# Optimization experiments

Hardware: AMD Instinct MI355X
Metric: run time of the kernel (lower is better)

The kernel has to match this reference:

```python
import jax, jax.numpy as jnp
import numpy as np

B_SZ, L_MAX, T_LEN, D = 512, 48, 128, 300   # sentences, graph slots, tokens, glove_dim
N_A, N_C = 2048, 2048                        # aspect rows, clause rows
H, TOP_K = 4, 96                             # attention heads, top-k over flattened LxL


def setup_inputs() -> dict:
    key = jax.random.key(0)
    ks = jax.random.split(key, 8)
    input_embed = jax.random.normal(ks[0], (B_SZ, T_LEN, D), jnp.float32)
    clause_output = jax.random.normal(ks[1], (N_C, D), jnp.float32)
    batch_aa_mask = (jax.random.uniform(ks[2], (N_A, T_LEN)) < 0.5).astype(jnp.float32)
    aa_graph_length = jax.random.randint(ks[3], (B_SZ,), 1, L_MAX + 1, dtype=jnp.int32)
    # collision-free scatter destinations; maxima hit B_SZ-1 and L_MAX-1 exactly
    map_AA = jnp.arange(N_A, dtype=jnp.int32) % B_SZ
    map_AA_idx = (4 + jnp.arange(N_A, dtype=jnp.int32) // B_SZ).at[-1].set(L_MAX - 1)
    map_AS = jnp.arange(N_C, dtype=jnp.int32) % B_SZ
    map_AS_idx = jnp.arange(N_C, dtype=jnp.int32) // B_SZ
    sc = 1.0 / np.sqrt(D).astype(np.float32)
    Wq = jax.random.normal(ks[4], (D, D), jnp.float32) * sc
    Wk = jax.random.normal(ks[5], (D, D), jnp.float32) * sc
    Wg = jax.random.normal(ks[6], (D, D), jnp.float32) * sc
    bq = jnp.zeros((D,), jnp.float32)
    bk = jnp.zeros((D,), jnp.float32)
    bg = jnp.zeros((D,), jnp.float32)
    return {"input_embed": input_embed, "clause_output": clause_output,
            "batch_aa_mask": batch_aa_mask, "aa_graph_length": aa_graph_length,
            "map_AA": map_AA, "map_AA_idx": map_AA_idx,
            "map_AS": map_AS, "map_AS_idx": map_AS_idx,
            "Wq": Wq, "bq": bq, "Wk": Wk, "bk": bk, "Wg": Wg, "bg": bg}


def reference(input_embed, clause_output, batch_aa_mask, aa_graph_length,
              map_AA, map_AA_idx, map_AS, map_AS_idx, Wq, bq, Wk, bk, Wg, bg):
    B, L = B_SZ, L_MAX
    dk = D // H
    # gather sentence tokens per aspect, masked sum over tokens -> [Na, D]
    aa_embed = jnp.einsum('ntd,nt->nd', input_embed[map_AA], batch_aa_mask)
    # scatter aspect and clause features into the [B, L, D] graph tensor
    inner = jnp.zeros((B, L, D), input_embed.dtype)
    inner = inner.at[map_AA, map_AA_idx].set(aa_embed)
    inner = inner.at[map_AS, map_AS_idx].set(clause_output)
    mask_indi = (jnp.arange(L)[None, :] < aa_graph_length[:, None]).astype(inner.dtype)  # [B,L]
    # attention-based adjacency (scores only, softmax over keys)
    q = (inner @ Wq.T + bq).reshape(B, L, H, dk).transpose(0, 2, 1, 3)
    k = (inner @ Wk.T + bk).reshape(B, L, H, dk).transpose(0, 2, 1, 3)
    scores = jnp.einsum('bhid,bhjd->bhij', q, k) / jnp.sqrt(jnp.asarray(dk, inner.dtype))
    scores = jnp.where(mask_indi[:, None, None, :] == 0, -1e9, scores)
    attn = jax.nn.softmax(scores, axis=-1)                      # [B,H,L,L]
    # average heads, replace diagonal with self-loops, zero padded rows
    adj = attn.mean(axis=1)
    eye = jnp.eye(L, dtype=adj.dtype)
    adj = adj * (1.0 - eye) + eye
    adj = adj * mask_indi[:, :, None]
    # top-k sparsify over flattened adjacency, symmetrize, diag=1, reweight
    flat = adj.reshape(B, L * L)
    kth = jax.lax.top_k(flat, TOP_K)[0][:, -1]                  # [B]
    sel = (flat >= kth[:, None]).astype(adj.dtype).reshape(B, L, L)
    sel = sel + sel.transpose(0, 2, 1)
    sel = sel * (1.0 - eye) + eye
    adj = sel * adj
    # one GCN layer: relu(W(A x) / (rowsum(A)+1))
    denom = adj.sum(axis=-1, keepdims=True) + 1.0
    gcn = jax.nn.relu((jnp.einsum('bij,bjd->bid', adj, inner) @ Wg.T + bg) / denom)
    # gather back to clause rows; keep clause_output where graph has <=1 node
    aa_out = gcn[map_AS, map_AS_idx]                            # [Nc, D]
    need = (aa_graph_length[map_AS] > 1)[:, None]
    return jnp.where(need, aa_out, clause_output)
```

## Files before the change

### kernel.cpp

```cpp
#include <hip/hip_runtime.h>
#include <math.h>

#define B_SZ 512
#define LG 48
#define T_LEN 128
#define DIM 300
#define NA 2048
#define NC 2048
#define NH 4
#define DK 75
#define KTOP 96
#define ACAP 16
#define TM 64
#define TN 64
#define KC 100
#define QKS 608
#define GTM 32
#define GTN 64
#define GKC 60
#define FCAP2 9
#define SSTR 612

__global__ __launch_bounds__(256) void build_kernel(
    const int* __restrict__ mapAA, const int* __restrict__ mapAAi,
    int* __restrict__ slot_src, int* __restrict__ acnt, int* __restrict__ alist) {
  int n = blockIdx.x * 256 + threadIdx.x;
  if (n >= NA) return;
  int b = mapAA[n];
  atomicMax(&slot_src[b * LG + mapAAi[n]], n);
  int pos = atomicAdd(&acnt[b], 1);
  if (pos < ACAP) alist[b * ACAP + pos] = n;
}

__global__ __launch_bounds__(256) void aspect_kernel(
    const float* __restrict__ embed, const float* __restrict__ mask,
    const int* __restrict__ acnt, const int* __restrict__ alist,
    float* __restrict__ X) {
  int b = blockIdx.x;
  int na = acnt[b]; if (na > ACAP) na = ACAP;
  if (na == 0) return;
  __shared__ float mLds[ACAP][T_LEN];
  __shared__ float4 eLds[32][DK];
  int tid = threadIdx.x;
  for (int i = tid; i < na * T_LEN; i += 256) {
    int k = i / T_LEN, t = i - k * T_LEN;
    mLds[k][t] = mask[(size_t)alist[b * ACAP + k] * T_LEN + t];
  }
  int nw = na * DK;
  int i0 = tid, i1 = tid + 256;
  int k0 = i0 / DK, d0 = i0 - k0 * DK;
  int k1 = i1 / DK, d1 = i1 - k1 * DK;
  float4 a0 = {0, 0, 0, 0}, a1 = {0, 0, 0, 0};
  const float4* e4 = (const float4*)(embed + (size_t)b * T_LEN * DIM);
  for (int t0 = 0; t0 < T_LEN; t0 += 32) {
    __syncthreads();
    for (int i = tid; i < 32 * DK; i += 256) {
      int t = i / DK, d = i - t * DK;
      eLds[t][d] = e4[(size_t)(t0 + t) * DK + d];
    }
    __syncthreads();
#pragma unroll
    for (int t = 0; t < 32; ++t) {
      if (i0 < nw) {
        float m = mLds[k0][t0 + t]; float4 ev = eLds[t][d0];
        a0.x += m * ev.x; a0.y += m * ev.y; a0.z += m * ev.z; a0.w += m * ev.w;
      }
      if (i1 < nw) {
        float m = mLds[k1][t0 + t]; float4 ev = eLds[t][d1];
        a1.x += m * ev.x; a1.y += m * ev.y; a1.z += m * ev.z; a1.w += m * ev.w;
      }
    }
  }
  if (i0 < nw) ((float4*)(X + (size_t)alist[b * ACAP + k0] * DIM))[d0] = a0;
  if (i1 < nw) ((float4*)(X + (size_t)alist[b * ACAP + k1] * DIM))[d1] = a1;
}

__global__ __launch_bounds__(128) void clause_kernel(
    const float* __restrict__ clause, const int* __restrict__ mapAS,
    const int* __restrict__ mapASi, float* __restrict__ X,
    int* __restrict__ slot_src) {
  int n = blockIdx.x, t = threadIdx.x;
  const float4* src = (const float4*)(clause + (size_t)n * DIM);
  float4* dst = (float4*)(X + (size_t)(NA + n) * DIM);
  if (t < DIM / 4) dst[t] = src[t];
  if (t == 96) atomicMax(&slot_src[mapAS[n] * LG + mapASi[n]], NA + n);
}

__global__ __launch_bounds__(256) void qk_kernel(
    const float* __restrict__ X, const float* __restrict__ Wq,
    const float* __restrict__ bq, const float* __restrict__ Wk,
    const float* __restrict__ bk, float* __restrict__ QK) {
  __shared__ __align__(16) float xs[TM][KC];
  __shared__ __align__(16) float ws[TN][KC];
  int m0 = blockIdx.x * TM, n0 = blockIdx.y * TN;
  int tid = threadIdx.x;
  int ty = tid >> 4;
  int tx = tid & 15;
  float acc[4][4];
#pragma unroll
  for (int a = 0; a < 4; ++a)
#pragma unroll
    for (int c = 0; c < 4; ++c) acc[a][c] = 0.f;

  for (int kc = 0; kc < DIM; kc += KC) {
    __syncthreads();
    for (int i = tid; i < TM * (KC / 4); i += 256) {
      int r = i / (KC / 4), g = i - r * (KC / 4);
      *(float4*)&xs[r][g * 4] =
          *(const float4*)&X[(size_t)(m0 + r) * DIM + kc + g * 4];
    }
    for (int i = tid; i < TN * (KC / 4); i += 256) {
      int c = i / (KC / 4), g = i - c * (KC / 4);
      int col = n0 + c;
      float4 v = {0.f, 0.f, 0.f, 0.f};
      if (col < 2 * DIM) {
        const float* w = (col < DIM) ? (Wq + (size_t)col * DIM)
                                     : (Wk + (size_t)(col - DIM) * DIM);
        v = *(const float4*)&w[kc + g * 4];
      }
      *(float4*)&ws[c][g * 4] = v;
    }
    __syncthreads();
#pragma unroll 5
    for (int kg = 0; kg < KC / 4; ++kg) {
      float4 xv[4], wv[4];
#pragma unroll
      for (int a = 0; a < 4; ++a) xv[a] = *(const float4*)&xs[ty * 4 + a][kg * 4];
#pragma unroll
      for (int c = 0; c < 4; ++c) wv[c] = *(const float4*)&ws[tx + 16 * c][kg * 4];
#pragma unroll
      for (int a = 0; a < 4; ++a)
#pragma unroll
        for (int c = 0; c < 4; ++c)
          acc[a][c] += wv[c].x * xv[a].x + wv[c].y * xv[a].y +
                       wv[c].z * xv[a].z + wv[c].w * xv[a].w;
    }
  }

#pragma unroll
  for (int cc = 0; cc < 4; ++cc) {
    int col = n0 + tx + 16 * cc;
    if (col < 2 * DIM) {
      float bias; int off;
      if (col < DIM) { bias = bq[col]; off = col + col / DK; }
      else { int c2 = col - DIM; bias = bk[c2]; off = 304 + c2 + c2 / DK; }
#pragma unroll
      for (int a = 0; a < 4; ++a)
        QK[(size_t)(m0 + ty * 4 + a) * QKS + off] = acc[a][cc] + bias;
    }
  }
}

__global__ __launch_bounds__(512) void attn2_kernel(
    const float* __restrict__ QK, const float* __restrict__ X,
    const float* __restrict__ bq, const float* __restrict__ bk,
    const int* __restrict__ slot_src, const int* __restrict__ aa_len,
    float* __restrict__ xout, float* __restrict__ dng, int* __restrict__ mdg) {
  int b = blockIdx.x, tid = threadIdx.x;
  __shared__ __align__(16) float staged[FCAP2][SSTR];
  __shared__ float buf4[NH][LG][LG + 1];
  __shared__ float coef[4][LG], denomc[4];
  __shared__ int srcs[LG], nlist[LG], flist[LG], qrow[LG];
  __shared__ float kthL;
  __shared__ int sh_nneed, sh_nf;

  int length = aa_len[b];
  if (length > LG) length = LG;
  if (tid < LG) srcs[tid] = slot_src[b * LG + tid];
  __syncthreads();

  if (tid < 64) {
    bool isneed = (tid < LG) && (srcs[tid] >= NA);
    unsigned long long nm = __ballot(isneed);
    if (isneed) nlist[__popcll(nm & ((1ull << tid) - 1ull))] = tid;
    bool isf = (tid < LG) && (srcs[tid] >= 0);
    unsigned long long fm = __ballot(isf);
    int nf = __popcll(fm);
    if (nf > FCAP2 - 1) nf = FCAP2 - 1;
    if (isf) {
      int c = __popcll(fm & ((1ull << tid) - 1ull));
      if (c < FCAP2 - 1) flist[c] = tid;
    }
    if (tid < LG) {
      int c = __popcll(fm & ((1ull << tid) - 1ull));
      qrow[tid] = (isf && c < FCAP2 - 1) ? c : nf;
    }
    if (tid == 0) { sh_nneed = __popcll(nm); sh_nf = nf; }
  }
  __syncthreads();
  int nneed = sh_nneed, nf = sh_nf;

  if (length <= 1) {
    if (tid < nneed) mdg[srcs[nlist[tid]] - NA] = 0;
    return;
  }

  for (int i = tid; i < nf * 152; i += 512) {
    int m = i / 152, g = i - m * 152;
    ((float4*)staged[m])[g] =
        ((const float4*)(QK + (size_t)srcs[flist[m]] * QKS))[g];
  }
  for (int j = tid; j < 608; j += 512) {
    int half = (j >= 304) ? 1 : 0;
    int jj = j - half * 304;
    int h = jj / 76, d = jj - h * 76;
    float v = 0.f;
    if (d < DK) v = half ? bk[h * DK + d] : bq[h * DK + d];
    staged[nf][j] = v;
  }
  __syncthreads();
  if (tid < nf * 8) {
    int m = tid >> 3, p = tid & 7;
    int pos = (p & 3) * 76 + 75 + ((p >> 2) * 304);
    staged[m][pos] = 0.f;
  }
  __syncthreads();

  const float sdk = sqrtf((float)DK);
  int h = tid >> 7;
  int t = tid & 127;
  int ti = t >> 3, tj = t & 7;
  int i0 = ti * 3, j0 = tj * 6;

  int qr[3], kr[6];
#pragma unroll
  for (int a = 0; a < 3; ++a) qr[a] = qrow[i0 + a];
#pragma unroll
  for (int c = 0; c < 6; ++c) kr[c] = qrow[j0 + c];

  if (i0 < length) {
    float acc[3][6];
#pragma unroll
    for (int a = 0; a < 3; ++a)
#pragma unroll
      for (int c = 0; c < 6; ++c) acc[a][c] = 0.f;
    for (int d4 = 0; d4 < 19; ++d4) {
      float4 qv[3], kv[6];
#pragma unroll
      for (int a = 0; a < 3; ++a)
        qv[a] = *(const float4*)&staged[qr[a]][h * 76 + d4 * 4];
#pragma unroll
      for (int c = 0; c < 6; ++c)
        kv[c] = *(const float4*)&staged[kr[c]][304 + h * 76 + d4 * 4];
#pragma unroll
      for (int a = 0; a < 3; ++a)
#pragma unroll
        for (int c = 0; c < 6; ++c)
          acc[a][c] += qv[a].x * kv[c].x + qv[a].y * kv[c].y +
                       qv[a].z * kv[c].z + qv[a].w * kv[c].w;
    }
#pragma unroll
    for (int a = 0; a < 3; ++a) {
      float p[6];
#pragma unroll
      for (int c = 0; c < 6; ++c)
        p[c] = (j0 + c < length) ? (acc[a][c] / sdk) : -1e9f;
      float mx = p[0];
#pragma unroll
      for (int c = 1; c < 6; ++c) mx = fmaxf(mx, p[c]);
      mx = fmaxf(mx, __shfl_xor(mx, 1));
      mx = fmaxf(mx, __shfl_xor(mx, 2));
      mx = fmaxf(mx, __shfl_xor(mx, 4));
      float rs = 0.f;
#pragma unroll
      for (int c = 0; c < 6; ++c) { p[c] = expf(p[c] - mx); rs += p[c]; }
      rs += __shfl_xor(rs, 1);
      rs += __shfl_xor(rs, 2);
      rs += __shfl_xor(rs, 4);
      if (i0 + a < length) {
#pragma unroll
        for (int c = 0; c < 6; ++c)
          buf4[h][i0 + a][j0 + c] = p[c] / rs;
      }
    }
  }
  __syncthreads();

  for (int e = tid; e < LG * LG; e += 512) {
    int i = e / LG, j = e - (e / LG) * LG;
    float v = 0.f;
    if (i < length)
      v = ((buf4[0][i][j] + buf4[1][i][j]) +
           (buf4[2][i][j] + buf4[3][i][j])) * 0.25f;
    if (i == j) v = (i < length) ? 1.0f : 0.0f;
    buf4[0][i][j] = v;
  }
  __syncthreads();

  if (tid < 64) {
    unsigned int vb[36];
#pragma unroll
    for (int v = 0; v < 36; ++v) {
      int e = v * 64 + tid;
      vb[v] = __float_as_uint(buf4[0][e / LG][e % LG]);
    }
    unsigned int cur = 0u;
    for (int bit = 30; bit >= 0; --bit) {
      unsigned int cand = cur | (1u << bit);
      int c = 0;
#pragma unroll
      for (int v = 0; v < 36; ++v) c += (vb[v] >= cand) ? 1 : 0;
      c += __shfl_xor(c, 32); c += __shfl_xor(c, 16);
      c += __shfl_xor(c, 8);  c += __shfl_xor(c, 4);
      c += __shfl_xor(c, 2);  c += __shfl_xor(c, 1);
      if (c >= KTOP) cur = cand;
    }
    if (tid == 0) kthL = __uint_as_float(cur);
  }
  __syncthreads();
  const float kth = kthL;

  int nc = (nneed > 4) ? 4 : nneed;
  if (tid < nc * LG) {
    int r = tid / LG, j = tid - (tid / LG) * LG;
    int i = nlist[r];
    float aij = buf4[0][i][j];
    float v;
    if (j == i) v = aij;
    else {
      float selv = (aij >= kth ? 1.f : 0.f) + (buf4[0][j][i] >= kth ? 1.f : 0.f);
      v = selv * aij;
    }
    coef[r][j] = v;
  }
  __syncthreads();
  if (tid < nc) {
    float sm = 0.f;
    for (int j = 0; j < LG; ++j) sm += coef[tid][j];
    denomc[tid] = sm + 1.f;
  }
  __syncthreads();
  for (int w = tid; w < nc * (DIM / 4); w += 512) {
    int r = w / (DIM / 4), d4 = w - (w / (DIM / 4)) * (DIM / 4);
    float4 acc = {0.f, 0.f, 0.f, 0.f};
    for (int m = 0; m < nf; ++m) {
      int j = flist[m];
      float a = coef[r][j];
      float4 xv = ((const float4*)(X + (size_t)srcs[j] * DIM))[d4];
      acc.x += a * xv.x; acc.y += a * xv.y;
      acc.z += a * xv.z; acc.w += a * xv.w;
    }
    int n = srcs[nlist[r]] - NA;
    ((float4*)(xout + (size_t)n * DIM))[d4] = acc;
  }
  if (tid < nc) {
    int n = srcs[nlist[tid]] - NA;
    mdg[n] = 1;
    dng[n] = denomc[tid];
  }
}

__global__ __launch_bounds__(256) void gcn_kernel(
    const float* __restrict__ xg, const float* __restrict__ dng,
    const int* __restrict__ mdg, const float* __restrict__ Wg,
    const float* __restrict__ bg, const float* __restrict__ clause,
    float* __restrict__ out) {
  __shared__ __align__(16) float xs[GTM][GKC];
  __shared__ __align__(16) float ws[GTN][GKC];
  int m0 = blockIdx.x * GTM, n0 = blockIdx.y * GTN;
  int tid = threadIdx.x;
  int ty = tid >> 4;
  int tx = tid & 15;
  float acc[2][4];
#pragma unroll
  for (int a = 0; a < 2; ++a)
#pragma unroll
    for (int c = 0; c < 4; ++c) acc[a][c] = 0.f;

  for (int kc = 0; kc < DIM; kc += GKC) {
    __syncthreads();
    for (int i = tid; i < GTM * (GKC / 4); i += 256) {
      int r = i / (GKC / 4), g = i - r * (GKC / 4);
      *(float4*)&xs[r][g * 4] =
          *(const float4*)&xg[(size_t)(m0 + r) * DIM + kc + g * 4];
    }
    for (int i = tid; i < GTN * (GKC / 4); i += 256) {
      int c = i / (GKC / 4), g = i - c * (GKC / 4);
      int col = n0 + c;
      float4 v = {0.f, 0.f, 0.f, 0.f};
      if (col < DIM)
        v = *(const float4*)&Wg[(size_t)col * DIM + kc + g * 4];
      *(float4*)&ws[c][g * 4] = v;
    }
    __syncthreads();
#pragma unroll 5
    for (int kg = 0; kg < GKC / 4; ++kg) {
      float4 xv[2], wv[4];
#pragma unroll
      for (int a = 0; a < 2; ++a) xv[a] = *(const float4*)&xs[ty * 2 + a][kg * 4];
#pragma unroll
      for (int c = 0; c < 4; ++c) wv[c] = *(const float4*)&ws[tx + 16 * c][kg * 4];
#pragma unroll
      for (int a = 0; a < 2; ++a)
#pragma unroll
        for (int c = 0; c < 4; ++c)
          acc[a][c] += wv[c].x * xv[a].x + wv[c].y * xv[a].y +
                       wv[c].z * xv[a].z + wv[c].w * xv[a].w;
    }
  }

  int md[2]; float dn[2];
#pragma unroll
  for (int a = 0; a < 2; ++a) {
    int row = m0 + ty * 2 + a;
    md[a] = mdg[row];
    dn[a] = dng[row];
  }
#pragma unroll
  for (int cc = 0; cc < 4; ++cc) {
    int col = n0 + tx + 16 * cc;
    if (col < DIM) {
      float bgc = bg[col];
#pragma unroll
      for (int a = 0; a < 2; ++a) {
        int row = m0 + ty * 2 + a;
        float v;
        if (md[a]) v = fmaxf((acc[a][cc] + bgc) / dn[a], 0.f);
        else v = clause[(size_t)row * DIM + col];
        out[(size_t)row * DIM + col] = v;
      }
    }
  }
}

extern "C" void kernel_launch(void* const* d_in, const int* in_sizes, int n_in,
                              void* d_out, int out_size, void* d_ws, size_t ws_size,
                              hipStream_t stream) {
  (void)in_sizes; (void)n_in; (void)out_size; (void)ws_size;
  const float* input_embed = (const float*)d_in[0];
  const float* clause      = (const float*)d_in[1];
  const float* aa_mask     = (const float*)d_in[2];
  const int*   aa_len      = (const int*)d_in[3];
  const int*   map_AA      = (const int*)d_in[4];
  const int*   map_AA_idx  = (const int*)d_in[5];
  const int*   map_AS      = (const int*)d_in[6];
  const int*   map_AS_idx  = (const int*)d_in[7];
  const float* Wq = (const float*)d_in[8];
  const float* bq = (const float*)d_in[9];
  const float* Wk = (const float*)d_in[10];
  const float* bk = (const float*)d_in[11];
  const float* Wg = (const float*)d_in[12];
  const float* bg = (const float*)d_in[13];
  float* out = (float*)d_out;

  float* X  = (float*)d_ws;
  float* QK = X + (size_t)(NA + NC) * DIM;
  int* slot_src = (int*)(QK + (size_t)(NA + NC) * QKS);
  int* acnt = slot_src + B_SZ * LG;
  int* alist = acnt + B_SZ;
  float* dng = (float*)alist;
  int* mdg = (int*)(dng + NC);
  float* xg = (float*)(alist + B_SZ * ACAP);

  hipMemsetAsync(slot_src, 0xFF, (size_t)B_SZ * LG * sizeof(int), stream);
  hipMemsetAsync(acnt, 0x00, (size_t)B_SZ * sizeof(int), stream);
  build_kernel<<<(NA + 255) / 256, 256, 0, stream>>>(map_AA, map_AA_idx,
                                                     slot_src, acnt, alist);
  clause_kernel<<<NC, 128, 0, stream>>>(clause, map_AS, map_AS_idx, X, slot_src);
  aspect_kernel<<<B_SZ, 256, 0, stream>>>(input_embed, aa_mask, acnt, alist, X);
  dim3 qkgrid((NA + NC) / TM, (2 * DIM + TN - 1) / TN);
  qk_kernel<<<qkgrid, 256, 0, stream>>>(X, Wq, bq, Wk, bk, QK);
  attn2_kernel<<<B_SZ, 512, 0, stream>>>(QK, X, bq, bk, slot_src, aa_len,
                                         xg, dng, mdg);
  dim3 ggrid(NC / GTM, (DIM + GTN - 1) / GTN);
  gcn_kernel<<<ggrid, 256, 0, stream>>>(xg, dng, mdg, Wg, bg, clause, out);
}
```

Baseline: 150.5 us.

## Compute attention per distinct row type and read X directly in QK GEMM

Measured after the change: 235.1 us. 1.56x slower.

```diff
diff --git a/kernel.cpp b/kernel.cpp
--- a/kernel.cpp
+++ b/kernel.cpp
@@ -20,6 +20,7 @@
 #define GKC 60
 #define FCAP2 9
 #define SSTR 612
+#define NTMAX 10
 
 __global__ __launch_bounds__(256) void build_kernel(
     const int* __restrict__ mapAA, const int* __restrict__ mapAAi,
@@ -90,7 +91,6 @@
     const float* __restrict__ X, const float* __restrict__ Wq,
     const float* __restrict__ bq, const float* __restrict__ Wk,
     const float* __restrict__ bk, float* __restrict__ QK) {
-  __shared__ __align__(16) float xs[TM][KC];
   __shared__ __align__(16) float ws[TN][KC];
   int m0 = blockIdx.x * TM, n0 = blockIdx.y * TN;
   int tid = threadIdx.x;
@@ -102,13 +102,12 @@
 #pragma unroll
     for (int c = 0; c < 4; ++c) acc[a][c] = 0.f;
 
+  const float* xrow[4];
+#pragma unroll
+  for (int a = 0; a < 4; ++a) xrow[a] = X + (size_t)(m0 + ty * 4 + a) * DIM;
+
   for (int kc = 0; kc < DIM; kc += KC) {
     __syncthreads();
-    for (int i = tid; i < TM * (KC / 4); i += 256) {
-      int r = i / (KC / 4), g = i - r * (KC / 4);
-      *(float4*)&xs[r][g * 4] =
-          *(const float4*)&X[(size_t)(m0 + r) * DIM + kc + g * 4];
-    }
     for (int i = tid; i < TN * (KC / 4); i += 256) {
       int c = i / (KC / 4), g = i - c * (KC / 4);
       int col = n0 + c;
@@ -125,7 +124,8 @@
     for (int kg = 0; kg < KC / 4; ++kg) {
       float4 xv[4], wv[4];
 #pragma unroll
-      for (int a = 0; a < 4; ++a) xv[a] = *(const float4*)&xs[ty * 4 + a][kg * 4];
+      for (int a = 0; a < 4; ++a)
+        xv[a] = *(const float4*)&xrow[a][kc + kg * 4];
 #pragma unroll
       for (int c = 0; c < 4; ++c) wv[c] = *(const float4*)&ws[tx + 16 * c][kg * 4];
 #pragma unroll
@@ -158,7 +158,8 @@
     float* __restrict__ xout, float* __restrict__ dng, int* __restrict__ mdg) {
   int b = blockIdx.x, tid = threadIdx.x;
   __shared__ __align__(16) float staged[FCAP2][SSTR];
-  __shared__ float buf4[NH][LG][LG + 1];
+  __shared__ float st[NH][NTMAX][LG + 1];
+  __shared__ float adj[LG][LG + 1];
   __shared__ float coef[4][LG], denomc[4];
   __shared__ int srcs[LG], nlist[LG], flist[LG], qrow[LG];
   __shared__ float kthL;
@@ -217,44 +218,35 @@
   __syncthreads();
 
   const float sdk = sqrtf((float)DK);
-  int h = tid >> 7;
-  int t = tid & 127;
-  int ti = t >> 3, tj = t & 7;
-  int i0 = ti * 3, j0 = tj * 6;
-
-  int qr[3], kr[6];
-#pragma unroll
-  for (int a = 0; a < 3; ++a) qr[a] = qrow[i0 + a];
-#pragma unroll
-  for (int c = 0; c < 6; ++c) kr[c] = qrow[j0 + c];
-
-  if (i0 < length) {
-    float acc[3][6];
-#pragma unroll
-    for (int a = 0; a < 3; ++a)
-#pragma unroll
-      for (int c = 0; c < 6; ++c) acc[a][c] = 0.f;
-    for (int d4 = 0; d4 < 19; ++d4) {
-      float4 qv[3], kv[6];
-#pragma unroll
-      for (int a = 0; a < 3; ++a)
-        qv[a] = *(const float4*)&staged[qr[a]][h * 76 + d4 * 4];
+  int ntypes = nf + 1;
+  {
+    int h = tid >> 7;
+    int t = tid & 127;
+    int tt = t >> 3;
+    int tj = t & 7;
+    int j0 = tj * 6;
+    if (tt < ntypes) {
+      int kr[6];
+#pragma unroll
+      for (int c = 0; c < 6; ++c) kr[c] = qrow[j0 + c];
+      float acc[6];
+#pragma unroll
+      for (int c = 0; c < 6; ++c) acc[c] = 0.f;
+      for (int d4 = 0; d4 < 19; ++d4) {
+        float4 qv = *(const float4*)&staged[tt][h * 76 + d4 * 4];
+        float4 kv[6];
+#pragma unroll
+        for (int c = 0; c < 6; ++c)
+          kv[c] = *(const float4*)&staged[kr[c]][304 + h * 76 + d4 * 4];
+#pragma unroll
+        for (int c = 0; c < 6; ++c)
+          acc[c] += qv.x * kv[c].x + qv.y * kv[c].y +
+                    qv.z * kv[c].z + qv.w * kv[c].w;
+      }
+      float p[6];
 #pragma unroll
       for (int c = 0; c < 6; ++c)
-        kv[c] = *(const float4*)&staged[kr[c]][304 + h * 76 + d4 * 4];
-#pragma unroll
-      for (int a = 0; a < 3; ++a)
-#pragma unroll
-        for (int c = 0; c < 6; ++c)
-          acc[a][c] += qv[a].x * kv[c].x + qv[a].y * kv[c].y +
-                       qv[a].z * kv[c].z + qv[a].w * kv[c].w;
-    }
-#pragma unroll
-    for (int a = 0; a < 3; ++a) {
-      float p[6];
-#pragma unroll
-      for (int c = 0; c < 6; ++c)
-        p[c] = (j0 + c < length) ? (acc[a][c] / sdk) : -1e9f;
+        p[c] = (j0 + c < length) ? (acc[c] / sdk) : -1e9f;
       float mx = p[0];
 #pragma unroll
       for (int c = 1; c < 6; ++c) mx = fmaxf(mx, p[c]);
@@ -267,11 +259,8 @@
       rs += __shfl_xor(rs, 1);
       rs += __shfl_xor(rs, 2);
       rs += __shfl_xor(rs, 4);
-      if (i0 + a < length) {
-#pragma unroll
-        for (int c = 0; c < 6; ++c)
-          buf4[h][i0 + a][j0 + c] = p[c] / rs;
-      }
+#pragma unroll
+      for (int c = 0; c < 6; ++c) st[h][tt][j0 + c] = p[c] / rs;
     }
   }
   __syncthreads();
@@ -279,11 +268,13 @@
   for (int e = tid; e < LG * LG; e += 512) {
     int i = e / LG, j = e - (e / LG) * LG;
     float v = 0.f;
-    if (i < length)
-      v = ((buf4[0][i][j] + buf4[1][i][j]) +
-           (buf4[2][i][j] + buf4[3][i][j])) * 0.25f;
+    if (i < length) {
+      int ty = qrow[i];
+      v = ((st[0][ty][j] + st[1][ty][j]) +
+           (st[2][ty][j] + st[3][ty][j])) * 0.25f;
+    }
     if (i == j) v = (i < length) ? 1.0f : 0.0f;
-    buf4[0][i][j] = v;
+    adj[i][j] = v;
   }
   __syncthreads();
 
@@ -292,7 +283,7 @@
 #pragma unroll
     for (int v = 0; v < 36; ++v) {
       int e = v * 64 + tid;
-      vb[v] = __float_as_uint(buf4[0][e / LG][e % LG]);
+      vb[v] = __float_as_uint(adj[e / LG][e % LG]);
     }
     unsigned int cur = 0u;
     for (int bit = 30; bit >= 0; --bit) {
@@ -314,11 +305,11 @@
   if (tid < nc * LG) {
     int r = tid / LG, j = tid - (tid / LG) * LG;
     int i = nlist[r];
-    float aij = buf4[0][i][j];
+    float aij = adj[i][j];
     float v;
     if (j == i) v = aij;
     else {
-      float selv = (aij >= kth ? 1.f : 0.f) + (buf4[0][j][i] >= kth ? 1.f : 0.f);
+      float selv = (aij >= kth ? 1.f : 0.f) + (adj[j][i] >= kth ? 1.f : 0.f);
       v = selv * aij;
     }
     coef[r][j] = v;
```
